# Kernel optimization log

Measured on AMD Instinct MI355X. Metric: run time of the kernel, lower is better.

## Reference

```python
import jax, jax.numpy as jnp
import numpy as np

MIN_POS = 1e-6
EPS = 1e-20
B, S, F_IN, E, H = 2, 1024, 768, 768, 12
DH = E // H   # nnmf in_features per head (64)
FH = E // H   # nnmf out_features per head (hidden_features=embed_dim default)
N_NNMF_ITERS = 3
N_ALPHA_ITERS = 3


def l1norm(x, axis=-1):
    # F.normalize(x, p=1, dim=axis, eps=1e-20) for non-negative x
    return x / jnp.maximum(jnp.sum(jnp.abs(x), axis=axis, keepdims=True), EPS)


def setup_inputs() -> dict:
    key = jax.random.key(0)
    k = jax.random.split(key, 6)
    return {
        "x": jax.random.normal(k[0], (B, S, F_IN), jnp.float32),
        "embed_w": jax.random.normal(k[1], (E, F_IN), jnp.float32) * 0.02,
        "embed_b": jnp.zeros((E,), jnp.float32),
        "nnmf_w": jax.random.uniform(k[2], (FH, DH), jnp.float32),  # non-negative NMF dictionary
        "out_w": jax.random.normal(k[3], (F_IN, E), jnp.float32) * 0.02,
        "out_b": jnp.zeros((F_IN,), jnp.float32),
    }


def reference(x, embed_w, embed_b, nnmf_w, out_w, out_b):
    # normalize NMF weight rows (p=1 over in_features), as nnmf_layer.normalize_weights
    W = nnmf_w / jnp.maximum(jnp.sum(nnmf_w, axis=1, keepdims=True), EPS)  # [FH, DH]

    # embed + clamp positive, split heads
    xe = jnp.clip(x @ embed_w.T + embed_b, MIN_POS)            # [B,S,E]
    xe = xe.reshape(B, S, H, DH)                                # [B,S,H,DH]

    # NNMFDense: prepared_input = l1-normalized input (normalize_input_dim=-1)
    inp = l1norm(xe)                                            # [B,S,H,DH]
    h = l1norm(jnp.ones((B, S, H, FH), x.dtype))                # init hidden
    rec = inp
    for _ in range(N_NNMF_ITERS):
        rec = l1norm(jnp.clip(h @ W, MIN_POS))                  # reconstruction [B,S,H,DH]
        h = l1norm(jnp.clip(h * ((inp / rec) @ W.T), MIN_POS))  # multiplicative update

    # normalize_h (p=1, dim=-1)
    h = l1norm(h)                                               # [B,S,H,FH] -> 'bohf'

    # alpha dynamics fixed point
    alpha = jnp.ones((B, H, S, S), x.dtype)                     # 'bhoi'
    h_rec_input = rec * inp                                     # [B,S,H,DH]
    for _ in range(N_ALPHA_ITERS):
        h_mixed = jnp.einsum('bohf,bhoi->bihf', h, alpha)       # [B,S,H,FH]
        arec_inv = 1.0 / (h_mixed @ W + EPS)                    # _reconstruct -> [B,S,H,DH]
        alpha = alpha * jnp.einsum('bohf,bihf->bhoi', h_rec_input, arec_inv)

    out = jnp.einsum('bohf,bhoi->bihf', h, alpha)               # [B,S,H,FH]
    out = out.reshape(B, S, E)                                  # flatten heads
    return out @ out_w.T + out_b                                # out_project
```

## Files before the change

kernel.cpp:

```cpp
#include <hip/hip_runtime.h>

#define B_  2
#define S_  1024
#define FIN 768
#define E_  768
#define H_  12
#define DH  64

typedef unsigned int uint;
typedef unsigned short ushort;
typedef __attribute__((ext_vector_type(8))) short short8;
typedef __attribute__((ext_vector_type(4))) float floatx4;

__device__ __forceinline__ ushort f2bf(float f) {
    uint u = __float_as_uint(f);
    return (ushort)((u + 0x7fffu + ((u >> 16) & 1u)) >> 16);
}

__device__ __forceinline__ uint4 pack8(const ushort* p) {
    uint4 r;
    r.x = (uint)p[0] | ((uint)p[1] << 16);
    r.y = (uint)p[2] | ((uint)p[3] << 16);
    r.z = (uint)p[4] | ((uint)p[5] << 16);
    r.w = (uint)p[6] | ((uint)p[7] << 16);
    return r;
}

__device__ __forceinline__ void split8v(float4 a, float4 b, short8& hi, short8& lo) {
    float v[8] = {a.x, a.y, a.z, a.w, b.x, b.y, b.z, b.w};
    ushort h[8], l[8];
#pragma unroll
    for (int j = 0; j < 8; ++j) {
        h[j] = f2bf(v[j]);
        l[j] = f2bf(v[j] - __uint_as_float(((uint)h[j]) << 16));
    }
    uint4 H = pack8(h), L = pack8(l);
    hi = *(short8*)&H;
    lo = *(short8*)&L;
}

__global__ __launch_bounds__(256) void k_conv(const float* __restrict__ xs,
                                              const float* __restrict__ ew,
                                              const float* __restrict__ nw,
                                              ushort* __restrict__ xsH,
                                              ushort* __restrict__ xsL,
                                              ushort* __restrict__ ewH,
                                              ushort* __restrict__ ewL,
                                              float* __restrict__ Wn,
                                              float* __restrict__ r1inv,
                                              ushort* __restrict__ Wfrag) {
    __shared__ float Wl[64 * 65];
    const int tid = threadIdx.x, bid = blockIdx.x;

    if (bid < 768) {
        const size_t i = ((size_t)bid * 256 + tid) * 8;
        short8 hi, lo;
        split8v(*(const float4*)(xs + i), *(const float4*)(xs + i + 4), hi, lo);
        *(short8*)(xsH + i) = hi;
        *(short8*)(xsL + i) = lo;
        return;
    }
    if (bid < 1056) {
        const size_t i = ((size_t)(bid - 768) * 256 + tid) * 8;
        short8 hi, lo;
        split8v(*(const float4*)(ew + i), *(const float4*)(ew + i + 4), hi, lo);
        *(short8*)(ewH + i) = hi;
        *(short8*)(ewL + i) = lo;
        return;
    }

    const int f = tid >> 2, q = tid & 3;
    float v[16];
    float s = 0.f;
#pragma unroll
    for (int i = 0; i < 16; ++i) { v[i] = nw[f * 64 + q * 16 + i]; s += v[i]; }
    s += __shfl_xor(s, 1, 64);
    s += __shfl_xor(s, 2, 64);
    const float inv = 1.f / fmaxf(s, 1e-20f);
    float w[16];
#pragma unroll
    for (int i = 0; i < 16; ++i) {
        w[i] = v[i] * inv;
        Wn[f * 64 + q * 16 + i] = w[i];
        Wl[f * 65 + q * 16 + i] = w[i];
    }
    __syncthreads();
    if (tid < 64) {
        float cs = 0.f;
        for (int ff = 0; ff < 64; ++ff) cs += Wl[ff * 65 + tid];
        float t = fmaxf(cs * (1.f / 64.f), 1e-6f);
        float S = t;
#pragma unroll
        for (int m = 1; m < 64; m <<= 1) S += __shfl_xor(S, m, 64);
        S = fmaxf(S, 1e-20f);
        r1inv[tid] = S / t;
    }
    {
        short8 h0, l0, h1, l1;
        split8v(make_float4(w[0], w[1], w[2], w[3]),
                make_float4(w[4], w[5], w[6], w[7]), h0, l0);
        split8v(make_float4(w[8], w[9], w[10], w[11]),
                make_float4(w[12], w[13], w[14], w[15]), h1, l1);
        ushort* WwH = Wfrag + 2 * 4096;
        ushort* WwL = Wfrag + 3 * 4096;
        *(short8*)(WwH + f * 64 + q * 16) = h0;
        *(short8*)(WwH + f * 64 + q * 16 + 8) = h1;
        *(short8*)(WwL + f * 64 + q * 16) = l0;
        *(short8*)(WwL + f * 64 + q * 16 + 8) = l1;
    }
    {
        float t[16];
#pragma unroll
        for (int i = 0; i < 16; ++i) t[i] = Wl[(q * 16 + i) * 65 + f];
        short8 h0, l0, h1, l1;
        split8v(make_float4(t[0], t[1], t[2], t[3]),
                make_float4(t[4], t[5], t[6], t[7]), h0, l0);
        split8v(make_float4(t[8], t[9], t[10], t[11]),
                make_float4(t[12], t[13], t[14], t[15]), h1, l1);
        ushort* WtH = Wfrag;
        ushort* WtL = Wfrag + 4096;
        *(short8*)(WtH + f * 64 + q * 16) = h0;
        *(short8*)(WtH + f * 64 + q * 16 + 8) = h1;
        *(short8*)(WtL + f * 64 + q * 16) = l0;
        *(short8*)(WtL + f * 64 + q * 16 + 8) = l1;
    }
}

__global__ __launch_bounds__(256) void k_embed(const ushort* __restrict__ xsH,
                                               const ushort* __restrict__ xsL,
                                               const ushort* __restrict__ ewH,
                                               const ushort* __restrict__ ewL,
                                               const float* __restrict__ eb,
                                               float* __restrict__ inp) {
    __shared__ __align__(16) unsigned char smem[28160];
    const int tid = threadIdx.x;
    const int bid = blockIdx.x;

    const int head = bid % 12;
    const int tok0 = (bid / 12) * 32;
    ushort* As_hi = (ushort*)smem;
    ushort* As_lo = As_hi + 32 * 72;
    ushort* Bs_hi = As_lo + 32 * 72;
    ushort* Bs_lo = Bs_hi + 64 * 72;
    float*  RS    = (float*)(Bs_lo + 64 * 72);

    const int wv = tid >> 6, lane = tid & 63;
    const int mbase = (wv >> 1) * 16;
    const int nbase = (wv & 1) * 32;
    const int lm = lane & 15, lq = lane >> 4;

    floatx4 accA[2], accB[2];
    accA[0] = (floatx4)0.f; accA[1] = (floatx4)0.f;
    accB[0] = (floatx4)0.f; accB[1] = (floatx4)0.f;

    const int arow = tid >> 3, akc = (tid & 7) * 8;
    const int brow = tid >> 2, bkq = (tid & 3) * 16;
    const ushort* xh = xsH + (size_t)(tok0 + arow) * FIN + akc;
    const ushort* xl = xsL + (size_t)(tok0 + arow) * FIN + akc;
    const ushort* wh = ewH + (size_t)(head * 64 + brow) * FIN + bkq;
    const ushort* wl = ewL + (size_t)(head * 64 + brow) * FIN + bkq;

    short8 pah, pal, pbh0, pbh1, pbl0, pbl1;
    pah  = *(const short8*)(xh);
    pal  = *(const short8*)(xl);
    pbh0 = *(const short8*)(wh);
    pbh1 = *(const short8*)(wh + 8);
    pbl0 = *(const short8*)(wl);
    pbl1 = *(const short8*)(wl + 8);

    for (int kb = 0; kb < FIN; kb += 64) {
        __syncthreads();
        {
            const int aoff = arow * 72 + akc;
            *(short8*)&As_hi[aoff] = pah;
            *(short8*)&As_lo[aoff] = pal;
            const int boff = brow * 72 + bkq;
            *(short8*)&Bs_hi[boff]     = pbh0;
            *(short8*)&Bs_hi[boff + 8] = pbh1;
            *(short8*)&Bs_lo[boff]     = pbl0;
            *(short8*)&Bs_lo[boff + 8] = pbl1;
        }
        __syncthreads();
        if (kb + 64 < FIN) {
            const int ko = kb + 64;
            pah  = *(const short8*)(xh + ko);
            pal  = *(const short8*)(xl + ko);
            pbh0 = *(const short8*)(wh + ko);
            pbh1 = *(const short8*)(wh + ko + 8);
            pbl0 = *(const short8*)(wl + ko);
            pbl1 = *(const short8*)(wl + ko + 8);
        }
#pragma unroll
        for (int ch = 0; ch < 2; ++ch) {
            const int ko = ch * 32 + lq * 8;
            short8 ah = *(const short8*)&As_hi[(mbase + lm) * 72 + ko];
            short8 al = *(const short8*)&As_lo[(mbase + lm) * 72 + ko];
#pragma unroll
            for (int ti = 0; ti < 2; ++ti) {
                short8 bh = *(const short8*)&Bs_hi[(nbase + ti * 16 + lm) * 72 + ko];
                short8 bl = *(const short8*)&Bs_lo[(nbase + ti * 16 + lm) * 72 + ko];
                accA[ti] = __builtin_amdgcn_mfma_f32_16x16x32_bf16(ah, bh, accA[ti], 0, 0, 0);
                accB[ti] = __builtin_amdgcn_mfma_f32_16x16x32_bf16(al, bh, accB[ti], 0, 0, 0);
                accB[ti] = __builtin_amdgcn_mfma_f32_16x16x32_bf16(ah, bl, accB[ti], 0, 0, 0);
            }
        }
    }

    const float b0 = eb[head * 64 + nbase + lm];
    const float b1 = eb[head * 64 + nbase + 16 + lm];
    float xe[2][4];
    float rs[4];
#pragma unroll
    for (int r = 0; r < 4; ++r) {
        float e0 = fmaxf((accA[0][r] + accB[0][r]) + b0, 1e-6f);
        float e1 = fmaxf((accA[1][r] + accB[1][r]) + b1, 1e-6f);
        xe[0][r] = e0; xe[1][r] = e1;
        float p = e0 + e1;
        p += __shfl_xor(p, 1, 64);
        p += __shfl_xor(p, 2, 64);
        p += __shfl_xor(p, 4, 64);
        p += __shfl_xor(p, 8, 64);
        rs[r] = p;
    }
    if (lm == 0) {
#pragma unroll
        for (int r = 0; r < 4; ++r)
            RS[(wv & 1) * 32 + mbase + lq * 4 + r] = rs[r];
    }
    __syncthreads();
    const size_t obase = ((size_t)((tok0 >> 10) * 12 + head) * 1024 + (tok0 & 1023));
#pragma unroll
    for (int r = 0; r < 4; ++r) {
        const int m = mbase + lq * 4 + r;
        const float inv = 1.f / fmaxf(RS[m] + RS[32 + m], 1e-20f);
        float* op = inp + (obase + m) * 64;
        op[nbase + lm]      = xe[0][r] * inv;
        op[nbase + 16 + lm] = xe[1][r] * inv;
    }
}

__device__ __forceinline__ void mfma_matvec(const float srcC[4][4], float* T,
                                            int lm, int lq,
                                            const ushort* WH, const ushort* WL,
                                            floatx4 out[4]) {
    __builtin_amdgcn_wave_barrier();
#pragma unroll
    for (int nt = 0; nt < 4; ++nt)
#pragma unroll
        for (int r = 0; r < 4; ++r)
            T[(lq * 4 + r) * 68 + nt * 16 + lm] = srcC[nt][r];
    __builtin_amdgcn_wave_barrier();
    float4 a00 = *(const float4*)&T[lm * 68 + lq * 8];
    float4 a01 = *(const float4*)&T[lm * 68 + lq * 8 + 4];
    float4 a10 = *(const float4*)&T[lm * 68 + 32 + lq * 8];
    float4 a11 = *(const float4*)&T[lm * 68 + 32 + lq * 8 + 4];
    __builtin_amdgcn_wave_barrier();
    short8 A0h, A0l, A1h, A1l;
    split8v(a00, a01, A0h, A0l);
    split8v(a10, a11, A1h, A1l);
#pragma unroll
    for (int nt = 0; nt < 4; ++nt) {
        const int row = (nt * 16 + lm) * 72;
        short8 b0h = *(const short8*)&WH[row + lq * 8];
        short8 b0l = *(const short8*)&WL[row + lq * 8];
        short8 b1h = *(const short8*)&WH[row + 32 + lq * 8];
        short8 b1l = *(const short8*)&WL[row + 32 + lq * 8];
        floatx4 acc0 = (floatx4)0.f, acc1 = (floatx4)0.f;
        acc0 = __builtin_amdgcn_mfma_f32_16x16x32_bf16(A0h, b0h, acc0, 0, 0, 0);
        acc0 = __builtin_amdgcn_mfma_f32_16x16x32_bf16(A0l, b0h, acc0, 0, 0, 0);
        acc0 = __builtin_amdgcn_mfma_f32_16x16x32_bf16(A0h, b0l, acc0, 0, 0, 0);
        acc1 = __builtin_amdgcn_mfma_f32_16x16x32_bf16(A1h, b1h, acc1, 0, 0, 0);
        acc1 = __builtin_amdgcn_mfma_f32_16x16x32_bf16(A1l, b1h, acc1, 0, 0, 0);
        acc1 = __builtin_amdgcn_mfma_f32_16x16x32_bf16(A1h, b1l, acc1, 0, 0, 0);
        out[nt] = acc0 + acc1;
    }
}

__global__ __launch_bounds__(256) void k_nnmf(const float* __restrict__ inp,
                                              const ushort* __restrict__ Wfrag,
                                              const float* __restrict__ r1inv,
                                              float* __restrict__ hout,
                                              float* __restrict__ hriout,
                                              float* __restrict__ mp0) {
    __shared__ ushort WtH[64 * 72], WtL[64 * 72];
    __shared__ ushort WwH[64 * 72], WwL[64 * 72];
    __shared__ float Tb[4][16 * 68];
    __shared__ float pbuf[256];
    const int tid = threadIdx.x, wv = tid >> 6, lane = tid & 63;
    const int lm = lane & 15, lq = lane >> 4;
    float* T = Tb[wv];
    const int rowbase = blockIdx.x * 64 + wv * 16;

    {
        const int row = tid >> 2, kq = (tid & 3) * 16;
        const int g = row * 64 + kq, l = row * 72 + kq;
        *(short8*)&WtH[l]     = *(const short8*)(Wfrag + g);
        *(short8*)&WtH[l + 8] = *(const short8*)(Wfrag + g + 8);
        *(short8*)&WtL[l]     = *(const short8*)(Wfrag + 4096 + g);
        *(short8*)&WtL[l + 8] = *(const short8*)(Wfrag + 4096 + g + 8);
        *(short8*)&WwH[l]     = *(const short8*)(Wfrag + 8192 + g);
        *(short8*)&WwH[l + 8] = *(const short8*)(Wfrag + 8192 + g + 8);
        *(short8*)&WwL[l]     = *(const short8*)(Wfrag + 12288 + g);
        *(short8*)&WwL[l + 8] = *(const short8*)(Wfrag + 12288 + g + 8);
    }

    float inpC[4][4];
#pragma unroll
    for (int nt = 0; nt < 4; ++nt)
#pragma unroll
        for (int r = 0; r < 4; ++r)
            inpC[nt][r] = inp[(size_t)(rowbase + lq * 4 + r) * 64 + nt * 16 + lm];
    float r1c[4];
#pragma unroll
    for (int nt = 0; nt < 4; ++nt) r1c[nt] = r1inv[nt * 16 + lm];
    __syncthreads();

    float hC[4][4], recC[4][4];
    {
        float qC[4][4];
#pragma unroll
        for (int nt = 0; nt < 4; ++nt)
#pragma unroll
            for (int r = 0; r < 4; ++r) qC[nt][r] = inpC[nt][r] * r1c[nt];
        floatx4 u[4];
        mfma_matvec(qC, T, lm, lq, WwH, WwL, u);
#pragma unroll
        for (int nt = 0; nt < 4; ++nt)
#pragma unroll
            for (int r = 0; r < 4; ++r)
                hC[nt][r] = fmaxf(u[nt][r] * (1.f / 64.f), 1e-6f);
#pragma unroll
        for (int r = 0; r < 4; ++r) {
            float s = (hC[0][r] + hC[1][r]) + (hC[2][r] + hC[3][r]);
            s += __shfl_xor(s, 1, 64); s += __shfl_xor(s, 2, 64);
            s += __shfl_xor(s, 4, 64); s += __shfl_xor(s, 8, 64);
            const float inv = __builtin_amdgcn_rcpf(fmaxf(s, 1e-20f));
#pragma unroll
            for (int nt = 0; nt < 4; ++nt) hC[nt][r] *= inv;
        }
    }
#pragma unroll 1
    for (int it = 0; it < 2; ++it) {
        floatx4 t[4];
        mfma_matvec(hC, T, lm, lq, WtH, WtL, t);
        float tC[4][4], qC[4][4];
#pragma unroll
        for (int nt = 0; nt < 4; ++nt)
#pragma unroll
            for (int r = 0; r < 4; ++r) tC[nt][r] = fmaxf(t[nt][r], 1e-6f);
#pragma unroll
        for (int r = 0; r < 4; ++r) {
            float s = (tC[0][r] + tC[1][r]) + (tC[2][r] + tC[3][r]);
            s += __shfl_xor(s, 1, 64); s += __shfl_xor(s, 2, 64);
            s += __shfl_xor(s, 4, 64); s += __shfl_xor(s, 8, 64);
            s = fmaxf(s, 1e-20f);
            const float invS = __builtin_amdgcn_rcpf(s);
#pragma unroll
            for (int nt = 0; nt < 4; ++nt) {
                recC[nt][r] = tC[nt][r] * invS;
                qC[nt][r] = inpC[nt][r] * s * __builtin_amdgcn_rcpf(tC[nt][r]);
            }
        }
        floatx4 u[4];
        mfma_matvec(qC, T, lm, lq, WwH, WwL, u);
#pragma unroll
        for (int nt = 0; nt < 4; ++nt)
#pragma unroll
            for (int r = 0; r < 4; ++r)
                hC[nt][r] = fmaxf(hC[nt][r] * u[nt][r], 1e-6f);
#pragma unroll
        for (int r = 0; r < 4; ++r) {
            float s = (hC[0][r] + hC[1][r]) + (hC[2][r] + hC[3][r]);
            s += __shfl_xor(s, 1, 64); s += __shfl_xor(s, 2, 64);
            s += __shfl_xor(s, 4, 64); s += __shfl_xor(s, 8, 64);
            const float inv = __builtin_amdgcn_rcpf(fmaxf(s, 1e-20f));
#pragma unroll
            for (int nt = 0; nt < 4; ++nt) hC[nt][r] *= inv;
        }
    }
#pragma unroll
    for (int r = 0; r < 4; ++r) {
        float s = (hC[0][r] + hC[1][r]) + (hC[2][r] + hC[3][r]);
        s += __shfl_xor(s, 1, 64); s += __shfl_xor(s, 2, 64);
        s += __shfl_xor(s, 4, 64); s += __shfl_xor(s, 8, 64);
        const float inv = __builtin_amdgcn_rcpf(fmaxf(s, 1e-20f));
#pragma unroll
        for (int nt = 0; nt < 4; ++nt) hC[nt][r] *= inv;
    }

#pragma unroll
    for (int nt = 0; nt < 4; ++nt)
#pragma unroll
        for (int r = 0; r < 4; ++r) {
            const size_t o = (size_t)(rowbase + lq * 4 + r) * 64 + nt * 16 + lm;
            hout[o] = hC[nt][r];
            hriout[o] = recC[nt][r] * inpC[nt][r];
        }

    float hs[4];
#pragma unroll
    for (int nt = 0; nt < 4; ++nt) {
        float s = (hC[nt][0] + hC[nt][1]) + (hC[nt][2] + hC[nt][3]);
        s += __shfl_xor(s, 16, 64);
        s += __shfl_xor(s, 32, 64);
        hs[nt] = s;
    }
    pbuf[wv * 64 + lq * 16 + lm] = hs[lq];
    __syncthreads();
    if (tid < 64) {
        float tot = (pbuf[tid] + pbuf[64 + tid]) + (pbuf[128 + tid] + pbuf[192 + tid]);
        mp0[(size_t)blockIdx.x * 64 + tid] = tot;
    }
}

__global__ __launch_bounds__(256) void k_alpha_step(const float* __restrict__ hin,
                                                    const float* __restrict__ hri,
                                                    const float* __restrict__ Wn,
                                                    const float* __restrict__ mp_in,
                                                    float* __restrict__ mp_out,
                                                    float* __restrict__ c,
                                                    int it) {
    __shared__ float mred[4][64];
    __shared__ float mv[64];
    __shared__ float vv[64];
    __shared__ float cl[64];
    const int tid = threadIdx.x;
    const int bh = blockIdx.x >> 4;
    const int chunk = blockIdx.x & 15;
    const size_t rowbase = (size_t)bh * 1024 + chunk * 64;

    {
        int f = tid & 63, p = tid >> 6;
        float s = 0.f;
#pragma unroll
        for (int pp = 0; pp < 4; ++pp)
            s += mp_in[((size_t)bh * 16 + p * 4 + pp) * 64 + f];
        mred[p][f] = s;
    }
    __syncthreads();
    if (tid < 64)
        mv[tid] = (mred[0][tid] + mred[1][tid]) + (mred[2][tid] + mred[3][tid]);
    __syncthreads();
    {
        int d = tid & 63, qq = tid >> 6;
        float r = 0.f;
#pragma unroll
        for (int ff = 0; ff < 16; ++ff)
            r = fmaf(mv[qq * 16 + ff], Wn[(size_t)(qq * 16 + ff) * 64 + d], r);
        mred[qq][d] = r;
    }
    __syncthreads();
    if (tid < 64)
        vv[tid] = 1.f / (((mred[0][tid] + mred[1][tid]) + (mred[2][tid] + mred[3][tid])) + 1e-20f);
    __syncthreads();
    {
        int o = tid >> 2, dq = tid & 3;
        const float* rp = hri + (rowbase + o) * 64 + dq * 16;
        float dot = 0.f;
#pragma unroll
        for (int t4 = 0; t4 < 16; t4 += 4) {
            float4 r4 = *(const float4*)(rp + t4);
            dot = fmaf(r4.x, vv[dq * 16 + t4 + 0], dot);
            dot = fmaf(r4.y, vv[dq * 16 + t4 + 1], dot);
            dot = fmaf(r4.z, vv[dq * 16 + t4 + 2], dot);
            dot = fmaf(r4.w, vv[dq * 16 + t4 + 3], dot);
        }
        dot += __shfl_xor(dot, 1, 64);
        dot += __shfl_xor(dot, 2, 64);
        float cn = dot;
        if (it >= 2) cn *= c[rowbase + o];
        if (dq == 0) { c[rowbase + o] = cn; cl[o] = cn; }
    }
    __syncthreads();
    {
        const int f4 = (tid & 15) * 4, ogr = tid >> 4;
        float4 a = make_float4(0.f, 0.f, 0.f, 0.f);
#pragma unroll
        for (int oi = 0; oi < 4; ++oi) {
            int o = ogr * 4 + oi;
            float4 h4 = *(const float4*)(hin + (rowbase + o) * 64 + f4);
            float cv = cl[o];
            a.x = fmaf(h4.x, cv, a.x); a.y = fmaf(h4.y, cv, a.y);
            a.z = fmaf(h4.z, cv, a.z); a.w = fmaf(h4.w, cv, a.w);
        }
        a.x += __shfl_xor(a.x, 16, 64); a.y += __shfl_xor(a.y, 16, 64);
        a.z += __shfl_xor(a.z, 16, 64); a.w += __shfl_xor(a.w, 16, 64);
        a.x += __shfl_xor(a.x, 32, 64); a.y += __shfl_xor(a.y, 32, 64);
        a.z += __shfl_xor(a.z, 32, 64); a.w += __shfl_xor(a.w, 32, 64);
        const int w = tid >> 6;
        if ((tid & 63) < 16) *(float4*)&mred[w][(tid & 15) * 4] = a;
    }
    __syncthreads();
    if (tid < 64) {
        float s = (mred[0][tid] + mred[1][tid]) + (mred[2][tid] + mred[3][tid]);
        mp_out[((size_t)bh * 16 + chunk) * 64 + tid] = s;
    }
}

__global__ __launch_bounds__(256) void k_projbcast(const float* __restrict__ mp3,
                                                   const float* __restrict__ ow,
                                                   const float* __restrict__ ob,
                                                   float* __restrict__ out) {
    __shared__ float Ml[768];
    __shared__ float ps[4][64];
    __shared__ float yseg[64];
    const int tid = threadIdx.x;
    const int b = blockIdx.x / 192;
    const int rem = blockIdx.x - b * 192;
    const int jt = rem >> 4, rg = rem & 15;
    for (int i = tid; i < 768; i += 256) {
        const int hh = i >> 6, f = i & 63;
        const float* src = mp3 + ((size_t)(b * 12 + hh) * 16) * 64 + f;
        float s = 0.f;
#pragma unroll
        for (int cc = 0; cc < 16; ++cc) s += src[cc * 64];
        Ml[i] = s;
    }
    __syncthreads();
    const int jj = tid & 63, part = tid >> 6;
    const int j = jt * 64 + jj;
    const float* row = ow + (size_t)j * 768 + part * 192;
    float acc = 0.f;
    for (int t = 0; t < 192; t += 4) {
        float4 w4 = *(const float4*)(row + t);
        acc = fmaf(w4.x, Ml[part * 192 + t + 0], acc);
        acc = fmaf(w4.y, Ml[part * 192 + t + 1], acc);
        acc = fmaf(w4.z, Ml[part * 192 + t + 2], acc);
        acc = fmaf(w4.w, Ml[part * 192 + t + 3], acc);
    }
    ps[part][jj] = acc;
    __syncthreads();
    if (tid < 64)
        yseg[tid] = ps[0][tid] + ps[1][tid] + ps[2][tid] + ps[3][tid] + ob[jt * 64 + tid];
    __syncthreads();
    const int r0 = tid >> 2, c4 = (tid & 3) * 16;
    float4 v4[4];
#pragma unroll
    for (int q = 0; q < 4; ++q) v4[q] = *(const float4*)&yseg[c4 + q * 4];
    float* dst = out + ((size_t)(b * 1024 + rg * 64 + r0)) * 768 + jt * 64 + c4;
#pragma unroll
    for (int q = 0; q < 4; ++q) *(float4*)(dst + q * 4) = v4[q];
}

extern "C" void kernel_launch(void* const* d_in, const int* in_sizes, int n_in,
                              void* d_out, int out_size, void* d_ws, size_t ws_size,
                              hipStream_t stream) {
    const float* xs = (const float*)d_in[0];
    const float* ew = (const float*)d_in[1];
    const float* eb = (const float*)d_in[2];
    const float* nw = (const float*)d_in[3];
    const float* ow = (const float*)d_in[4];
    const float* ob = (const float*)d_in[5];
    float* out = (float*)d_out;

    float* ws    = (float*)d_ws;
    float* inp   = ws;
    float* h     = ws + 1572864;
    float* hri   = ws + 3145728;
    float* Wn    = ws + 4718592;
    float* r1inv = ws + 4722688;
    float* mp0   = ws + 4722944;
    float* mp1   = ws + 4747520;
    float* mp2   = ws + 4772096;
    float* c     = ws + 4796672;
    ushort* xsH  = (ushort*)(ws + 4821248);
    ushort* xsL  = (ushort*)(ws + 5607680);
    ushort* ewH  = (ushort*)(ws + 6394112);
    ushort* ewL  = (ushort*)(ws + 6689024);
    ushort* Wfrag= (ushort*)(ws + 6983936);

    k_conv<<<1057, 256, 0, stream>>>(xs, ew, nw, xsH, xsL, ewH, ewL, Wn, r1inv, Wfrag);
    k_embed<<<768, 256, 0, stream>>>(xsH, xsL, ewH, ewL, eb, inp);
    k_nnmf<<<384, 256, 0, stream>>>(inp, Wfrag, r1inv, h, hri, mp0);
    k_alpha_step<<<384, 256, 0, stream>>>(h, hri, Wn, mp0, mp1, c, 1);
    k_alpha_step<<<384, 256, 0, stream>>>(h, hri, Wn, mp1, mp2, c, 2);
    k_alpha_step<<<384, 256, 0, stream>>>(h, hri, Wn, mp2, mp1, c, 3);
    k_projbcast<<<384, 256, 0, stream>>>(mp1, ow, ob, out);
}
```

Measured before the change: 131.5 us.

## Load embed GEMM MFMA fragments directly from global memory, dropping LDS staging

The embed GEMM kernel no longer stages the x and weight tiles through shared memory with double barriers per K step. Each wave now loads its MFMA operand fragments straight from global memory with 16-byte loads, and the loop over K is unrolled by four. This removes the LDS writes, LDS reads and __syncthreads, and shrinks shared memory to a small row-sum buffer, which may raise occupancy. In exchange, operands shared across waves are fetched redundantly from global memory or cache, and the per-lane 16-byte loads strided across rows coalesce less well.

```diff
diff --git a/kernel.cpp b/kernel.cpp
--- a/kernel.cpp
+++ b/kernel.cpp
@@ -132,17 +132,12 @@
                                                const ushort* __restrict__ ewL,
                                                const float* __restrict__ eb,
                                                float* __restrict__ inp) {
-    __shared__ __align__(16) unsigned char smem[28160];
+    __shared__ float RS[64];
     const int tid = threadIdx.x;
     const int bid = blockIdx.x;
 
     const int head = bid % 12;
     const int tok0 = (bid / 12) * 32;
-    ushort* As_hi = (ushort*)smem;
-    ushort* As_lo = As_hi + 32 * 72;
-    ushort* Bs_hi = As_lo + 32 * 72;
-    ushort* Bs_lo = Bs_hi + 64 * 72;
-    float*  RS    = (float*)(Bs_lo + 64 * 72);
 
     const int wv = tid >> 6, lane = tid & 63;
     const int mbase = (wv >> 1) * 16;
@@ -153,57 +148,30 @@
     accA[0] = (floatx4)0.f; accA[1] = (floatx4)0.f;
     accB[0] = (floatx4)0.f; accB[1] = (floatx4)0.f;
 
-    const int arow = tid >> 3, akc = (tid & 7) * 8;
-    const int brow = tid >> 2, bkq = (tid & 3) * 16;
-    const ushort* xh = xsH + (size_t)(tok0 + arow) * FIN + akc;
-    const ushort* xl = xsL + (size_t)(tok0 + arow) * FIN + akc;
-    const ushort* wh = ewH + (size_t)(head * 64 + brow) * FIN + bkq;
-    const ushort* wl = ewL + (size_t)(head * 64 + brow) * FIN + bkq;
-
-    short8 pah, pal, pbh0, pbh1, pbl0, pbl1;
-    pah  = *(const short8*)(xh);
-    pal  = *(const short8*)(xl);
-    pbh0 = *(const short8*)(wh);
-    pbh1 = *(const short8*)(wh + 8);
-    pbl0 = *(const short8*)(wl);
-    pbl1 = *(const short8*)(wl + 8);
-
-    for (int kb = 0; kb < FIN; kb += 64) {
-        __syncthreads();
-        {
-            const int aoff = arow * 72 + akc;
-            *(short8*)&As_hi[aoff] = pah;
-            *(short8*)&As_lo[aoff] = pal;
-            const int boff = brow * 72 + bkq;
-            *(short8*)&Bs_hi[boff]     = pbh0;
-            *(short8*)&Bs_hi[boff + 8] = pbh1;
-            *(short8*)&Bs_lo[boff]     = pbl0;
-            *(short8*)&Bs_lo[boff + 8] = pbl1;
-        }
-        __syncthreads();
-        if (kb + 64 < FIN) {
-            const int ko = kb + 64;
-            pah  = *(const short8*)(xh + ko);
-            pal  = *(const short8*)(xl + ko);
-            pbh0 = *(const short8*)(wh + ko);
-            pbh1 = *(const short8*)(wh + ko + 8);
-            pbl0 = *(const short8*)(wl + ko);
-            pbl1 = *(const short8*)(wl + ko + 8);
-        }
-#pragma unroll
-        for (int ch = 0; ch < 2; ++ch) {
-            const int ko = ch * 32 + lq * 8;
-            short8 ah = *(const short8*)&As_hi[(mbase + lm) * 72 + ko];
-            short8 al = *(const short8*)&As_lo[(mbase + lm) * 72 + ko];
-#pragma unroll
-            for (int ti = 0; ti < 2; ++ti) {
-                short8 bh = *(const short8*)&Bs_hi[(nbase + ti * 16 + lm) * 72 + ko];
-                short8 bl = *(const short8*)&Bs_lo[(nbase + ti * 16 + lm) * 72 + ko];
-                accA[ti] = __builtin_amdgcn_mfma_f32_16x16x32_bf16(ah, bh, accA[ti], 0, 0, 0);
-                accB[ti] = __builtin_amdgcn_mfma_f32_16x16x32_bf16(al, bh, accB[ti], 0, 0, 0);
-                accB[ti] = __builtin_amdgcn_mfma_f32_16x16x32_bf16(ah, bl, accB[ti], 0, 0, 0);
-            }
-        }
+    const size_t xrow = (size_t)(tok0 + mbase + lm) * FIN;
+    const size_t w0row = (size_t)(head * 64 + nbase + lm) * FIN;
+    const size_t w1row = (size_t)(head * 64 + nbase + 16 + lm) * FIN;
+    const ushort* xh  = xsH + xrow + lq * 8;
+    const ushort* xl  = xsL + xrow + lq * 8;
+    const ushort* w0h = ewH + w0row + lq * 8;
+    const ushort* w0l = ewL + w0row + lq * 8;
+    const ushort* w1h = ewH + w1row + lq * 8;
+    const ushort* w1l = ewL + w1row + lq * 8;
+
+#pragma unroll 4
+    for (int k0 = 0; k0 < FIN; k0 += 32) {
+        short8 ah  = *(const short8*)(xh + k0);
+        short8 al  = *(const short8*)(xl + k0);
+        short8 b0h = *(const short8*)(w0h + k0);
+        short8 b0l = *(const short8*)(w0l + k0);
+        short8 b1h = *(const short8*)(w1h + k0);
+        short8 b1l = *(const short8*)(w1l + k0);
+        accA[0] = __builtin_amdgcn_mfma_f32_16x16x32_bf16(ah, b0h, accA[0], 0, 0, 0);
+        accB[0] = __builtin_amdgcn_mfma_f32_16x16x32_bf16(al, b0h, accB[0], 0, 0, 0);
+        accB[0] = __builtin_amdgcn_mfma_f32_16x16x32_bf16(ah, b0l, accB[0], 0, 0, 0);
+        accA[1] = __builtin_amdgcn_mfma_f32_16x16x32_bf16(ah, b1h, accA[1], 0, 0, 0);
+        accB[1] = __builtin_amdgcn_mfma_f32_16x16x32_bf16(al, b1h, accB[1], 0, 0, 0);
+        accB[1] = __builtin_amdgcn_mfma_f32_16x16x32_bf16(ah, b1l, accB[1], 0, 0, 0);
     }
 
     const float b0 = eb[head * 64 + nbase + lm];
```

New measurement: 164.8 us. 1.25x slower.
